# Kernel optimization log

Measured on AMD Instinct MI355X. Metric: run time of the kernel, lower is better.

The kernel has to match this reference:

```python
import jax, jax.numpy as jnp
import numpy as np

B, S, D, H = 8, 1024, 512, 8  # batch, max_mol_real, d_model, num_heads
DH = D // 2                   # per-branch width
DEPTH = D // H                # per-head depth (64)
HH = H // 2                   # heads per branch (4)


def setup_inputs() -> dict:
    key = jax.random.key(0)
    ks = jax.random.split(key, 16)
    sc = 0.02
    inp = {
        'x': jax.random.normal(ks[0], (B, S, D), jnp.float32),
        'mask': jnp.zeros((B, 1, 1, S), jnp.float32),
        'adj': jax.random.uniform(ks[1], (B, S, S), jnp.float32),
        'dist': jax.random.uniform(ks[2], (B, S, S), jnp.float32),
        # dist branch projections (Dense(d_model/2))
        'Wq_dist': jax.random.normal(ks[3], (D, DH), jnp.float32) * sc,
        'bq_dist': jnp.zeros((DH,), jnp.float32),
        'Wk_dist': jax.random.normal(ks[4], (D, DH), jnp.float32) * sc,
        'bk_dist': jnp.zeros((DH,), jnp.float32),
        'Wv_dist': jax.random.normal(ks[5], (D, DH), jnp.float32) * sc,
        'bv_dist': jnp.zeros((DH,), jnp.float32),
        # adj branch projections
        'Wq_adj': jax.random.normal(ks[6], (D, DH), jnp.float32) * sc,
        'bq_adj': jnp.zeros((DH,), jnp.float32),
        'Wk_adj': jax.random.normal(ks[7], (D, DH), jnp.float32) * sc,
        'bk_adj': jnp.zeros((DH,), jnp.float32),
        'Wv_adj': jax.random.normal(ks[8], (D, DH), jnp.float32) * sc,
        'bv_adj': jnp.zeros((DH,), jnp.float32),
        # output projection Dense(d_model)
        'Wo': jax.random.normal(ks[9], (D, D), jnp.float32) * sc,
        'bo': jnp.zeros((D,), jnp.float32),
    }
    return inp


def _split_heads(t):
    # (B, S, HH*DEPTH) -> (B, HH, S, DEPTH)
    return t.reshape(B, S, HH, DEPTH).transpose(0, 2, 1, 3)


def _sdpa_ad(q, k, v, mask, adj=None, dist=None):
    # mask: (B,1,1,S) -> additive -1e9 * mask, per original code
    m = mask * -1000000000.0
    logits = jnp.einsum('bhqd,bhkd->bhqk', q, k) / jnp.sqrt(jnp.float32(DEPTH))
    w = jax.nn.softmax(logits + m, axis=-1)  # (B, HH, S, S)
    if adj is not None:
        w = w * adj[:, None, :, :]
    if dist is not None:  # dist_value == 'original'
        w = w * jax.nn.softmax(dist[:, None, :, :] + m, axis=-1)
    return jnp.einsum('bhqk,bhkd->bhqd', w, v)


def reference(x, mask, adj, dist,
              Wq_dist, bq_dist, Wk_dist, bk_dist, Wv_dist, bv_dist,
              Wq_adj, bq_adj, Wk_adj, bk_adj, Wv_adj, bv_adj,
              Wo, bo):
    # ----- dist branch -----
    qd = _split_heads(x @ Wq_dist + bq_dist)
    kd = _split_heads(x @ Wk_dist + bk_dist)
    vd = _split_heads(x @ Wv_dist + bv_dist)
    od = _sdpa_ad(qd, kd, vd, mask, adj=None, dist=dist)
    od = od.transpose(0, 2, 1, 3).reshape(B, S, DH)
    # ----- adj branch -----
    qa = _split_heads(x @ Wq_adj + bq_adj)
    ka = _split_heads(x @ Wk_adj + bk_adj)
    va = _split_heads(x @ Wv_adj + bv_adj)
    oa = _sdpa_ad(qa, ka, va, mask, adj=adj, dist=None)
    oa = oa.transpose(0, 2, 1, 3).reshape(B, S, DH)
    # ----- concat + output dense -----
    cat = jnp.concatenate([od, oa], axis=-1)  # (B, S, D)
    return cat @ Wo + bo
```

## Files before the change

kernel.cpp:

```cpp
#include <hip/hip_runtime.h>

typedef __attribute__((ext_vector_type(8))) short bf16x8;
typedef __attribute__((ext_vector_type(4))) float f32x4;
typedef __attribute__((ext_vector_type(4))) unsigned u32x4;
typedef unsigned short ushortT;

#define B_   8
#define S_   1024
#define D_   512
#define DH_  256
#define NH_  4
#define DEP_ 64
#define LOG2E 1.4426950408889634f

__device__ __forceinline__ unsigned short f2bf(float f){
    unsigned u = __builtin_bit_cast(unsigned, f);
    u += 0x7fffu + ((u>>16)&1u);
    return (unsigned short)(u>>16);
}
__device__ __forceinline__ float bf2f(ushortT v){
    unsigned u = ((unsigned)v)<<16;
    return __builtin_bit_cast(float, u);
}
__device__ __forceinline__ unsigned fbits(float f){ return __builtin_bit_cast(unsigned, f); }
__device__ __forceinline__ int swz(int row,int cb){ return (row<<7) + (cb ^ ((row&7)<<4)); }
__device__ __forceinline__ int sigrow(int sr){
    return 16*((sr>>5) + 2*((sr>>2)&1)) + 4*((sr>>3)&3) + (sr&3);
}
__device__ __forceinline__ void gload_lds16(const void* g, void* l){
    __builtin_amdgcn_global_load_lds(
        (const __attribute__((address_space(1))) unsigned*)(size_t)g,
        (__attribute__((address_space(3))) unsigned*)(unsigned)(size_t)l,
        16, 0, 0);
}

__global__ __launch_bounds__(256) void mega_prep(
    const float* __restrict__ x, ushortT* __restrict__ xb,
    const float* __restrict__ W0, const float* __restrict__ W1, const float* __restrict__ W2,
    const float* __restrict__ W3, const float* __restrict__ W4, const float* __restrict__ W5,
    const float* __restrict__ B0, const float* __restrict__ B1, const float* __restrict__ B2,
    const float* __restrict__ B3, const float* __restrict__ B4, const float* __restrict__ B5,
    ushortT* __restrict__ Wt, float* __restrict__ bias_all,
    const float* __restrict__ dist, const float* __restrict__ mask, ushortT* __restrict__ Md)
{
    __shared__ ushortT pl[16][1032];
    const int bid = blockIdx.x;
    if (bid < 4096){
        size_t t = (size_t)bid*256 + threadIdx.x;
        float4 v = *(const float4*)(x + t*4);
        ushort4 o; o.x=f2bf(v.x); o.y=f2bf(v.y); o.z=f2bf(v.z); o.w=f2bf(v.w);
        *(ushort4*)(xb + t*4) = o;
        return;
    }
    if (bid < 4864){
        int t = (bid-4096)*256 + threadIdx.x;
        int k = t / 384;
        int n4 = (t - k*384)*4;
#pragma unroll
        for (int j=0;j<4;++j){
            int n = n4+j; int mat = n>>8, nc = n&255;
            const float* Wp = (mat==0)?W0:(mat==1)?W1:(mat==2)?W2:(mat==3)?W3:(mat==4)?W4:W5;
            Wt[(size_t)n*512 + k] = f2bf(Wp[(size_t)k*256 + nc]);
        }
        if (t < 384){
#pragma unroll
            for (int j=0;j<4;++j){
                int n = n4+j; int mat = n>>8, nc = n&255;
                const float* Bp = (mat==0)?B0:(mat==1)?B1:(mat==2)?B2:(mat==3)?B3:(mat==4)?B4:B5;
                bias_all[n] = Bp[nc];
            }
        }
        return;
    }
    const int bx = bid - 4864;
    const int w = bx&3, qb = (bx>>2)&15, b = bx>>6;
    const int wd = threadIdx.x>>6, lane = threadIdx.x&63;
    const float* mrow = mask + (size_t)b*S_;

    for (int rr=0; rr<4; ++rr){
        const int er = 4*wd + rr;
        const int q = qb*64 + 16*w + er;
        const float* drow = dist + ((size_t)(b*1024 + q))*S_;
        float v[16];
        float mx = -1e30f;
#pragma unroll
        for (int j=0;j<4;++j){
            const int idx = j*256 + lane*4;
            float4 d = *(const float4*)(drow + idx);
            float4 mk = *(const float4*)(mrow + idx);
            v[j*4+0] = fmaf(mk.x, -1e9f, d.x); v[j*4+1] = fmaf(mk.y, -1e9f, d.y);
            v[j*4+2] = fmaf(mk.z, -1e9f, d.z); v[j*4+3] = fmaf(mk.w, -1e9f, d.w);
#pragma unroll
            for (int i=0;i<4;++i) mx = fmaxf(mx, v[j*4+i]);
        }
        mx = fmaxf(mx, __shfl_xor(mx,1));  mx = fmaxf(mx, __shfl_xor(mx,2));
        mx = fmaxf(mx, __shfl_xor(mx,4));  mx = fmaxf(mx, __shfl_xor(mx,8));
        mx = fmaxf(mx, __shfl_xor(mx,16)); mx = fmaxf(mx, __shfl_xor(mx,32));
        float s = 0.f;
#pragma unroll
        for (int i=0;i<16;++i){ v[i] = __builtin_exp2f((v[i]-mx)*LOG2E); s += v[i]; }
        s += __shfl_xor(s,1);  s += __shfl_xor(s,2);  s += __shfl_xor(s,4);
        s += __shfl_xor(s,8);  s += __shfl_xor(s,16); s += __shfl_xor(s,32);
        const float rcp = 1.f/s;
#pragma unroll
        for (int j=0;j<4;++j){
            ushort4 o;
            o.x=f2bf(v[j*4+0]*rcp); o.y=f2bf(v[j*4+1]*rcp);
            o.z=f2bf(v[j*4+2]*rcp); o.w=f2bf(v[j*4+3]*rcp);
            *(ushort4*)(&pl[er][j*256 + lane*4]) = o;
        }
    }
    __syncthreads();

    const int t = threadIdx.x;
    const int e2 = (t>>2)&15, kt2 = t&3, g2 = t>>6;
    const int koff = 32*(kt2&1) + 4*(kt2>>1) + 8*g2;
    ushortT* slab = Md + (((size_t)(b*16+qb)*16)*4 + w)*1024;
#pragma unroll
    for (int s2=0;s2<16;++s2){
        ushort4 vv = *(const ushort4*)(&pl[e2][64*s2 + koff]);
        *(ushort4*)(slab + (size_t)s2*4096 + t*4) = vv;
    }
}

__global__ __launch_bounds__(256) void prep_wo(const float* __restrict__ Wo, ushortT* __restrict__ Wot){
    __shared__ float t[32][33];
    const int k0 = blockIdx.y*32, n0 = blockIdx.x*32;
    const int ty = threadIdx.x>>5, tx = threadIdx.x&31;
#pragma unroll
    for (int i=0;i<4;++i)
        t[ty+8*i][tx] = Wo[(size_t)(k0+ty+8*i)*512 + n0+tx];
    __syncthreads();
#pragma unroll
    for (int i=0;i<4;++i)
        Wot[(size_t)(n0+ty+8*i)*512 + k0+tx] = f2bf(t[tx][ty+8*i]);
}

__global__ __launch_bounds__(256) void shuf_adj(
    const float* __restrict__ adj, ushortT* __restrict__ Ma)
{
    __shared__ ushortT tl[64][72];
    const int bx = blockIdx.x;
    const int s = bx&15, qb = (bx>>4)&15, b = bx>>8;
    const int t = threadIdx.x;
    {
        const int qr = t>>2, c0 = (t&3)*16;
        const float* src = adj + ((size_t)(b*1024 + qb*64 + qr))*S_ + 64*s + c0;
#pragma unroll
        for (int i=0;i<4;++i){
            float4 d = *(const float4*)(src + 4*i);
            tl[qr][c0+4*i+0]=f2bf(d.x); tl[qr][c0+4*i+1]=f2bf(d.y);
            tl[qr][c0+4*i+2]=f2bf(d.z); tl[qr][c0+4*i+3]=f2bf(d.w);
        }
    }
    __syncthreads();
    const int w2 = t>>6, l = t&63, g = l>>4, e = l&15;
    ushortT o[16];
#pragma unroll
    for (int kt=0;kt<4;++kt)
        *(ushort4*)(&o[4*kt]) = *(const ushort4*)(&tl[16*w2 + e][32*(kt&1) + 4*(kt>>1) + 8*g]);
    ushortT* dst = Ma + ((((size_t)(b*16+qb)*16 + s)*4 + w2)*1024) + l*16;
    *(uint4*)(dst)     = *(uint4*)(&o[0]);
    *(uint4*)(dst + 8) = *(uint4*)(&o[8]);
}

__global__ __launch_bounds__(256) void qkv_mfma(
    const ushortT* __restrict__ xb, const ushortT* __restrict__ Wt,
    const float* __restrict__ bias_all,
    ushortT* __restrict__ q_d, ushortT* __restrict__ k_d, ushortT* __restrict__ vt_d,
    ushortT* __restrict__ q_a, ushortT* __restrict__ k_a, ushortT* __restrict__ vt_a)
{
    __shared__ __align__(16) char sm[32768];
    const int tid = threadIdx.x;
    const int w = tid>>6, l = tid&63, g = l>>4, e = l&15;
    const int wm = w>>1, wn = w&1;
    const int n0 = blockIdx.x*128, m0 = blockIdx.y*128;

    f32x4 acc[4][4];
#pragma unroll
    for (int i=0;i<4;++i)
#pragma unroll
        for (int j=0;j<4;++j) acc[i][j] = (f32x4){0.f,0.f,0.f,0.f};

    for (int k0=0;k0<512;k0+=64){
        __syncthreads();
#pragma unroll
        for (int i=0;i<4;++i){
            const int ch  = w*256 + i*64 + l;
            const int row = ch>>3;
            const int cb  = (ch&7)*16;
            const int gc  = (cb ^ ((row&7)<<4)) >> 1;
            gload_lds16(xb + (size_t)(m0+row)*512 + k0 + gc, sm + (w*4096 + i*1024));
            gload_lds16(Wt + (size_t)(n0+row)*512 + k0 + gc, sm + 16384 + (w*4096 + i*1024));
        }
        __syncthreads();
#pragma unroll
        for (int c=0;c<2;++c){
            bf16x8 a[4];
#pragma unroll
            for (int mt=0;mt<4;++mt)
                a[mt] = *(const bf16x8*)(sm + swz(64*wm + 16*mt + e, g*16 + 64*c));
#pragma unroll
            for (int nt=0;nt<4;++nt){
                bf16x8 bfr = *(const bf16x8*)(sm + 16384 + swz(64*wn + 16*nt + e, g*16 + 64*c));
#pragma unroll
                for (int mt=0;mt<4;++mt)
                    acc[mt][nt] = __builtin_amdgcn_mfma_f32_16x16x32_bf16(a[mt], bfr, acc[mt][nt], 0,0,0);
            }
        }
    }

    const int mat = n0>>8;
    const int nb  = n0 + 64*wn;
    const int h   = (nb&255)>>6;
    const int mb  = m0 + 64*wm;
    const int b   = mb>>10, s0 = mb&1023;
    ushortT* base = (mat==0)?q_d:(mat==1)?k_d:(mat==2)?vt_d:(mat==3)?q_a:(mat==4)?k_a:vt_a;
    const bool isV = (mat==2)||(mat==5);

    float bi[4];
#pragma unroll
    for (int nt=0;nt<4;++nt) bi[nt] = bias_all[nb + 16*nt + e];

    __syncthreads();
    char* qd = sm + w*8192;
#pragma unroll
    for (int nt=0;nt<4;++nt){
#pragma unroll
        for (int mt=0;mt<4;++mt){
#pragma unroll
            for (int r=0;r<4;++r){
                const int row = 16*mt + 4*g + r;
                const int col = 16*nt + e;
                const int lr = isV ? col : row;
                const int lc = isV ? row : col;
                *(ushortT*)(qd + swz(lr, lc*2)) = f2bf(acc[mt][nt][r] + bi[nt]);
            }
        }
    }
    const int rrb = l>>3, dq = l&7;
#pragma unroll
    for (int pass=0;pass<8;++pass){
        const int rr = pass*8 + rrb;
        uint4 vv = *(const uint4*)(qd + swz(rr, dq*16));
        const size_t off = isV ? ((size_t)((b*NH_+h)*DEP_ + rr)*S_ + s0 + dq*8)
                               : ((size_t)((b*NH_+h)*S_ + s0 + rr)*DEP_ + dq*8);
        *(uint4*)(base + off) = vv;
    }
}

__global__ __launch_bounds__(256,4) void attn_mfma(
    const ushortT* __restrict__ q_d, const ushortT* __restrict__ k_d, const ushortT* __restrict__ vt_d,
    const ushortT* __restrict__ q_a, const ushortT* __restrict__ k_a, const ushortT* __restrict__ vt_a,
    const ushortT* __restrict__ Md, const ushortT* __restrict__ Ma,
    const float* __restrict__ mask, ushortT* __restrict__ cat)
{
    __shared__ __align__(16) char sm[20480];
    float* Msk = (float*)(sm + 16384);

    const int tid = threadIdx.x;
    const int w = tid>>6, l = tid&63, g = l>>4, e = l&15;
    const int bz = blockIdx.y;
    const int br = bz>>5;
    const int bh = bz&31, b = bh>>2, h = bh&3;
    const int qb = blockIdx.x;
    const int q0 = qb*64;

    const ushortT* Qg = br ? q_a  : q_d;
    const ushortT* Kg = br ? k_a  : k_d;
    const ushortT* Vg = br ? vt_a : vt_d;

    const ushortT* Qb = Qg + ((size_t)bh*S_ + q0)*DEP_;
    const ushortT* Kb = Kg + (size_t)bh*S_*DEP_;
    const ushortT* Vb = Vg + (size_t)bh*DEP_*S_;
    const ushortT* Mbase = (br ? Ma : Md) + ((size_t)((b*16+qb)*16)*4 + w)*1024 + l*16;
    const float*   mkb = mask + (size_t)b*S_;

    const int srow = tid>>3, sf = tid&7;
    const int srow2 = srow+32;
    const int krow  = sigrow(srow);
    const int krow2 = sigrow(srow2);

    bf16x8 aq0 = *(const bf16x8*)(Qb + (size_t)(16*w+e)*DEP_ + 8*g);
    bf16x8 aq1 = *(const bf16x8*)(Qb + (size_t)(16*w+e)*DEP_ + 8*g + 32);

    for (int i=tid;i<S_;i+=256) Msk[i] = mkb[i] * (-1e9f*LOG2E);

    uint4 kreg0 = *(const uint4*)(Kb + (size_t)srow*DEP_ + 8*sf);
    uint4 kreg1 = *(const uint4*)(Kb + (size_t)srow2*DEP_ + 8*sf);
    uint4 vreg0 = *(const uint4*)(Vb + (size_t)srow*S_  + 8*sf);
    uint4 vreg1 = *(const uint4*)(Vb + (size_t)srow2*S_ + 8*sf);
    bf16x8 mc0 = *(const bf16x8*)(Mbase);
    bf16x8 mc1 = *(const bf16x8*)(Mbase + 8);

    float zl = 0.f;
    f32x4 oacc[4];
#pragma unroll
    for (int dt=0;dt<4;++dt) oacc[dt] = (f32x4){0.f,0.f,0.f,0.f};

    for (int s=0;s<16;++s){
        const int k0 = s*64;
        __syncthreads();
        *(uint4*)(sm +        swz(krow,  sf*16)) = kreg0;
        *(uint4*)(sm +        swz(krow2, sf*16)) = kreg1;
        *(uint4*)(sm + 8192 + swz(srow,  sf*16)) = vreg0;
        *(uint4*)(sm + 8192 + swz(srow2, sf*16)) = vreg1;
        __syncthreads();

        const int kn = (s<15) ? k0+64 : 0;
        kreg0 = *(const uint4*)(Kb + (size_t)(kn+srow)*DEP_ + 8*sf);
        kreg1 = *(const uint4*)(Kb + (size_t)(kn+srow2)*DEP_ + 8*sf);
        vreg0 = *(const uint4*)(Vb + (size_t)srow*S_  + kn + 8*sf);
        vreg1 = *(const uint4*)(Vb + (size_t)srow2*S_ + kn + 8*sf);
        const size_t mo = (size_t)((s<15)?s+1:0)*4096;
        bf16x8 mn0 = *(const bf16x8*)(Mbase + mo);
        bf16x8 mn1 = *(const bf16x8*)(Mbase + mo + 8);

        f32x4 lg[4];
#pragma unroll
        for (int kt=0;kt<4;++kt) lg[kt] = (f32x4){0.f,0.f,0.f,0.f};
        __builtin_amdgcn_s_setprio(1);
#pragma unroll
        for (int kt=0;kt<4;++kt){
            bf16x8 bk0 = *(const bf16x8*)(sm + swz(16*kt + e, g*16));
            bf16x8 bk1 = *(const bf16x8*)(sm + swz(16*kt + e, g*16 + 64));
            lg[kt] = __builtin_amdgcn_mfma_f32_16x16x32_bf16(bk0, aq0, lg[kt], 0,0,0);
            lg[kt] = __builtin_amdgcn_mfma_f32_16x16x32_bf16(bk1, aq1, lg[kt], 0,0,0);
        }
        __builtin_amdgcn_s_setprio(0);

        unsigned pw[8];
#pragma unroll
        for (int kt=0;kt<4;++kt){
            const f32x4 mskv = *(const f32x4*)(Msk + k0 + 32*(kt&1) + 4*(kt>>1) + 8*g);
            float e1[4], pm[4];
#pragma unroll
            for (int r=0;r<4;++r)
                e1[r] = __builtin_exp2f(fmaf(lg[kt][r], 0.125f*LOG2E, mskv[r]));
            zl += (e1[0]+e1[1]) + (e1[2]+e1[3]);
#pragma unroll
            for (int r=0;r<4;++r){
                const int j = 4*kt + r;
                const float mj = bf2f((ushortT)(j<8 ? mc0[j] : mc1[j-8]));
                pm[r] = e1[r]*mj;
            }
            pw[2*kt]   = __builtin_amdgcn_perm(fbits(pm[1]), fbits(pm[0]), 0x07060302u);
            pw[2*kt+1] = __builtin_amdgcn_perm(fbits(pm[3]), fbits(pm[2]), 0x07060302u);
        }
        mc0 = mn0; mc1 = mn1;

        const bf16x8 ap0 = __builtin_bit_cast(bf16x8, (u32x4){pw[0],pw[1],pw[4],pw[5]});
        const bf16x8 ap1 = __builtin_bit_cast(bf16x8, (u32x4){pw[2],pw[3],pw[6],pw[7]});

        __builtin_amdgcn_s_setprio(1);
#pragma unroll
        for (int dt=0;dt<4;++dt){
            bf16x8 bv0 = *(const bf16x8*)(sm + 8192 + swz(16*dt + e, g*16));
            oacc[dt] = __builtin_amdgcn_mfma_f32_16x16x32_bf16(ap0, bv0, oacc[dt], 0,0,0);
        }
#pragma unroll
        for (int dt=0;dt<4;++dt){
            bf16x8 bv1 = *(const bf16x8*)(sm + 8192 + swz(16*dt + e, g*16 + 64));
            oacc[dt] = __builtin_amdgcn_mfma_f32_16x16x32_bf16(ap1, bv1, oacc[dt], 0,0,0);
        }
        __builtin_amdgcn_s_setprio(0);
    }

    zl += __shfl_xor(zl,16); zl += __shfl_xor(zl,32);
    float inv[4];
#pragma unroll
    for (int r=0;r<4;++r)
        inv[r] = 1.f / __shfl(zl, (l & 48) | (4*g + r));

    const int coff = br*DH_;
#pragma unroll
    for (int dt=0;dt<4;++dt){
#pragma unroll
        for (int r=0;r<4;++r){
            int q = q0 + 16*w + 4*g + r;
            int c = coff + h*DEP_ + 16*dt + e;
            cat[((size_t)b*S_ + q)*D_ + c] = f2bf(oacc[dt][r]*inv[r]);
        }
    }
}

__global__ __launch_bounds__(256) void out_mfma(
    const ushortT* __restrict__ catb, const ushortT* __restrict__ Wot,
    const float* __restrict__ bo, float* __restrict__ out)
{
    __shared__ __align__(16) char sm[16384];
    const int tid = threadIdx.x;
    const int w = tid>>6, l = tid&63, g = l>>4, e = l&15;
    const int n0 = blockIdx.x*64, m0 = blockIdx.y*64;

    f32x4 acc[4];
#pragma unroll
    for (int j=0;j<4;++j) acc[j] = (f32x4){0.f,0.f,0.f,0.f};

    for (int k0=0;k0<512;k0+=64){
        __syncthreads();
#pragma unroll
        for (int i=0;i<2;++i){
            int fi = tid + i*256;
            int row = fi>>3, f = fi&7;
            *(uint4*)(sm + swz(row, f*16))        = *(const uint4*)(catb + ((size_t)(m0+row)*512 + k0 + 8*f));
            *(uint4*)(sm + 8192 + swz(row, f*16)) = *(const uint4*)(Wot  + ((size_t)(n0+row)*512 + k0 + 8*f));
        }
        __syncthreads();
#pragma unroll
        for (int c=0;c<2;++c){
            bf16x8 a = *(const bf16x8*)(sm + swz(16*w + e, g*16 + 64*c));
#pragma unroll
            for (int nt=0;nt<4;++nt){
                bf16x8 bfr = *(const bf16x8*)(sm + 8192 + swz(16*nt + e, g*16 + 64*c));
                acc[nt] = __builtin_amdgcn_mfma_f32_16x16x32_bf16(a, bfr, acc[nt], 0,0,0);
            }
        }
    }

#pragma unroll
    for (int nt=0;nt<4;++nt){
        const int n = n0 + 16*nt + e;
        const float bi = bo[n];
#pragma unroll
        for (int r=0;r<4;++r){
            const int m = m0 + 16*w + 4*g + r;
            out[(size_t)m*512 + n] = acc[nt][r] + bi;
        }
    }
}

extern "C" void kernel_launch(void* const* d_in, const int* in_sizes, int n_in,
                              void* d_out, int out_size, void* d_ws, size_t ws_size,
                              hipStream_t stream)
{
    (void)in_sizes; (void)n_in; (void)out_size; (void)ws_size;

    const float* x    = (const float*)d_in[0];
    const float* mask = (const float*)d_in[1];
    const float* adj  = (const float*)d_in[2];
    const float* dist = (const float*)d_in[3];
    const float* Wqd  = (const float*)d_in[4];  const float* bqd = (const float*)d_in[5];
    const float* Wkd  = (const float*)d_in[6];  const float* bkd = (const float*)d_in[7];
    const float* Wvd  = (const float*)d_in[8];  const float* bvd = (const float*)d_in[9];
    const float* Wqa  = (const float*)d_in[10]; const float* bqa = (const float*)d_in[11];
    const float* Wka  = (const float*)d_in[12]; const float* bka = (const float*)d_in[13];
    const float* Wva  = (const float*)d_in[14]; const float* bva = (const float*)d_in[15];
    const float* Wo   = (const float*)d_in[16]; const float* bo  = (const float*)d_in[17];
    float* out = (float*)d_out;

    char* W = (char*)d_ws;
    ushortT* xb   = (ushortT*)(W + 0);
    ushortT* catb = (ushortT*)(W + 0);
    ushortT* Wt   = (ushortT*)(W + 8388608);
    ushortT* Ma   = (ushortT*)(W + 8388608);
    ushortT* Wot  = (ushortT*)(W + 8388608);
    float*   bias = (float*)  (W + 9961472);
    ushortT* q_d  = (ushortT*)(W + 25165824);
    ushortT* k_d  = (ushortT*)(W + 29360128);
    ushortT* vt_d = (ushortT*)(W + 33554432);
    ushortT* q_a  = (ushortT*)(W + 37748736);
    ushortT* k_a  = (ushortT*)(W + 41943040);
    ushortT* vt_a = (ushortT*)(W + 46137344);
    ushortT* Md   = (ushortT*)(W + 50331648);

    mega_prep<<<5376, 256, 0, stream>>>(x, xb,
        Wqd,Wkd,Wvd,Wqa,Wka,Wva, bqd,bkd,bvd,bqa,bka,bva, Wt, bias,
        dist, mask, Md);
    qkv_mfma<<<dim3(12,64), 256, 0, stream>>>(xb, Wt, bias, q_d,k_d,vt_d, q_a,k_a,vt_a);
    shuf_adj<<<2048, 256, 0, stream>>>(adj, Ma);
    attn_mfma<<<dim3(16,64), 256, 0, stream>>>(q_d,k_d,vt_d, q_a,k_a,vt_a,
                                               Md, Ma, mask, catb);
    prep_wo<<<dim3(16,16), 256, 0, stream>>>(Wo, Wot);
    out_mfma<<<dim3(8,128), 256, 0, stream>>>(catb, Wot, bo, out);
}
```

Measured before the change: 113.3 us.

## Read adj directly as fp32 in attention and fold Wo transpose into prep

```diff
diff --git a/kernel.cpp b/kernel.cpp
--- a/kernel.cpp
+++ b/kernel.cpp
@@ -41,9 +41,11 @@
     const float* __restrict__ B0, const float* __restrict__ B1, const float* __restrict__ B2,
     const float* __restrict__ B3, const float* __restrict__ B4, const float* __restrict__ B5,
     ushortT* __restrict__ Wt, float* __restrict__ bias_all,
-    const float* __restrict__ dist, const float* __restrict__ mask, ushortT* __restrict__ Md)
+    const float* __restrict__ dist, const float* __restrict__ mask, ushortT* __restrict__ Md,
+    const float* __restrict__ Wo, ushortT* __restrict__ Wot)
 {
     __shared__ ushortT pl[16][1032];
+    __shared__ float tt[32][33];
     const int bid = blockIdx.x;
     if (bid < 4096){
         size_t t = (size_t)bid*256 + threadIdx.x;
@@ -72,96 +74,70 @@
         }
         return;
     }
-    const int bx = bid - 4864;
-    const int w = bx&3, qb = (bx>>2)&15, b = bx>>6;
-    const int wd = threadIdx.x>>6, lane = threadIdx.x&63;
-    const float* mrow = mask + (size_t)b*S_;
-
-    for (int rr=0; rr<4; ++rr){
-        const int er = 4*wd + rr;
-        const int q = qb*64 + 16*w + er;
-        const float* drow = dist + ((size_t)(b*1024 + q))*S_;
-        float v[16];
-        float mx = -1e30f;
-#pragma unroll
-        for (int j=0;j<4;++j){
-            const int idx = j*256 + lane*4;
-            float4 d = *(const float4*)(drow + idx);
-            float4 mk = *(const float4*)(mrow + idx);
-            v[j*4+0] = fmaf(mk.x, -1e9f, d.x); v[j*4+1] = fmaf(mk.y, -1e9f, d.y);
-            v[j*4+2] = fmaf(mk.z, -1e9f, d.z); v[j*4+3] = fmaf(mk.w, -1e9f, d.w);
-#pragma unroll
-            for (int i=0;i<4;++i) mx = fmaxf(mx, v[j*4+i]);
-        }
-        mx = fmaxf(mx, __shfl_xor(mx,1));  mx = fmaxf(mx, __shfl_xor(mx,2));
-        mx = fmaxf(mx, __shfl_xor(mx,4));  mx = fmaxf(mx, __shfl_xor(mx,8));
-        mx = fmaxf(mx, __shfl_xor(mx,16)); mx = fmaxf(mx, __shfl_xor(mx,32));
-        float s = 0.f;
-#pragma unroll
-        for (int i=0;i<16;++i){ v[i] = __builtin_exp2f((v[i]-mx)*LOG2E); s += v[i]; }
-        s += __shfl_xor(s,1);  s += __shfl_xor(s,2);  s += __shfl_xor(s,4);
-        s += __shfl_xor(s,8);  s += __shfl_xor(s,16); s += __shfl_xor(s,32);
-        const float rcp = 1.f/s;
-#pragma unroll
-        for (int j=0;j<4;++j){
-            ushort4 o;
-            o.x=f2bf(v[j*4+0]*rcp); o.y=f2bf(v[j*4+1]*rcp);
-            o.z=f2bf(v[j*4+2]*rcp); o.w=f2bf(v[j*4+3]*rcp);
-            *(ushort4*)(&pl[er][j*256 + lane*4]) = o;
-        }
-    }
-    __syncthreads();
-
-    const int t = threadIdx.x;
-    const int e2 = (t>>2)&15, kt2 = t&3, g2 = t>>6;
-    const int koff = 32*(kt2&1) + 4*(kt2>>1) + 8*g2;
-    ushortT* slab = Md + (((size_t)(b*16+qb)*16)*4 + w)*1024;
-#pragma unroll
-    for (int s2=0;s2<16;++s2){
-        ushort4 vv = *(const ushort4*)(&pl[e2][64*s2 + koff]);
-        *(ushort4*)(slab + (size_t)s2*4096 + t*4) = vv;
-    }
-}
-
-__global__ __launch_bounds__(256) void prep_wo(const float* __restrict__ Wo, ushortT* __restrict__ Wot){
-    __shared__ float t[32][33];
-    const int k0 = blockIdx.y*32, n0 = blockIdx.x*32;
-    const int ty = threadIdx.x>>5, tx = threadIdx.x&31;
-#pragma unroll
-    for (int i=0;i<4;++i)
-        t[ty+8*i][tx] = Wo[(size_t)(k0+ty+8*i)*512 + n0+tx];
-    __syncthreads();
-#pragma unroll
-    for (int i=0;i<4;++i)
-        Wot[(size_t)(n0+ty+8*i)*512 + k0+tx] = f2bf(t[tx][ty+8*i]);
-}
-
-__global__ __launch_bounds__(256) void shuf_adj(
-    const float* __restrict__ adj, ushortT* __restrict__ Ma)
-{
-    __shared__ ushortT tl[64][72];
-    const int bx = blockIdx.x;
-    const int s = bx&15, qb = (bx>>4)&15, b = bx>>8;
-    const int t = threadIdx.x;
+    if (bid < 5376){
+        const int bx = bid - 4864;
+        const int w = bx&3, qb = (bx>>2)&15, b = bx>>6;
+        const int wd = threadIdx.x>>6, lane = threadIdx.x&63;
+        const float* mrow = mask + (size_t)b*S_;
+
+        for (int rr=0; rr<4; ++rr){
+            const int er = 4*wd + rr;
+            const int q = qb*64 + 16*w + er;
+            const float* drow = dist + ((size_t)(b*1024 + q))*S_;
+            float v[16];
+            float mx = -1e30f;
+#pragma unroll
+            for (int j=0;j<4;++j){
+                const int idx = j*256 + lane*4;
+                float4 d = *(const float4*)(drow + idx);
+                float4 mk = *(const float4*)(mrow + idx);
+                v[j*4+0] = fmaf(mk.x, -1e9f, d.x); v[j*4+1] = fmaf(mk.y, -1e9f, d.y);
+                v[j*4+2] = fmaf(mk.z, -1e9f, d.z); v[j*4+3] = fmaf(mk.w, -1e9f, d.w);
+#pragma unroll
+                for (int i=0;i<4;++i) mx = fmaxf(mx, v[j*4+i]);
+            }
+            mx = fmaxf(mx, __shfl_xor(mx,1));  mx = fmaxf(mx, __shfl_xor(mx,2));
+            mx = fmaxf(mx, __shfl_xor(mx,4));  mx = fmaxf(mx, __shfl_xor(mx,8));
+            mx = fmaxf(mx, __shfl_xor(mx,16)); mx = fmaxf(mx, __shfl_xor(mx,32));
+            float s = 0.f;
+#pragma unroll
+            for (int i=0;i<16;++i){ v[i] = __builtin_exp2f((v[i]-mx)*LOG2E); s += v[i]; }
+            s += __shfl_xor(s,1);  s += __shfl_xor(s,2);  s += __shfl_xor(s,4);
+            s += __shfl_xor(s,8);  s += __shfl_xor(s,16); s += __shfl_xor(s,32);
+            const float rcp = 1.f/s;
+#pragma unroll
+            for (int j=0;j<4;++j){
+                ushort4 o;
+                o.x=f2bf(v[j*4+0]*rcp); o.y=f2bf(v[j*4+1]*rcp);
+                o.z=f2bf(v[j*4+2]*rcp); o.w=f2bf(v[j*4+3]*rcp);
+                *(ushort4*)(&pl[er][j*256 + lane*4]) = o;
+            }
+        }
+        __syncthreads();
+
+        const int t = threadIdx.x;
+        const int e2 = (t>>2)&15, kt2 = t&3, g2 = t>>6;
+        const int koff = 32*(kt2&1) + 4*(kt2>>1) + 8*g2;
+        ushortT* slab = Md + (((size_t)(b*16+qb)*16)*4 + w)*1024;
+#pragma unroll
+        for (int s2=0;s2<16;++s2){
+            ushort4 vv = *(const ushort4*)(&pl[e2][64*s2 + koff]);
+            *(ushort4*)(slab + (size_t)s2*4096 + t*4) = vv;
+        }
+        return;
+    }
     {
-        const int qr = t>>2, c0 = (t&3)*16;
-        const float* src = adj + ((size_t)(b*1024 + qb*64 + qr))*S_ + 64*s + c0;
-#pragma unroll
-        for (int i=0;i<4;++i){
-            float4 d = *(const float4*)(src + 4*i);
-            tl[qr][c0+4*i+0]=f2bf(d.x); tl[qr][c0+4*i+1]=f2bf(d.y);
-            tl[qr][c0+4*i+2]=f2bf(d.z); tl[qr][c0+4*i+3]=f2bf(d.w);
-        }
-    }
-    __syncthreads();
-    const int w2 = t>>6, l = t&63, g = l>>4, e = l&15;
-    ushortT o[16];
-#pragma unroll
-    for (int kt=0;kt<4;++kt)
-        *(ushort4*)(&o[4*kt]) = *(const ushort4*)(&tl[16*w2 + e][32*(kt&1) + 4*(kt>>1) + 8*g]);
-    ushortT* dst = Ma + ((((size_t)(b*16+qb)*16 + s)*4 + w2)*1024) + l*16;
-    *(uint4*)(dst)     = *(uint4*)(&o[0]);
-    *(uint4*)(dst + 8) = *(uint4*)(&o[8]);
+        const int bid2 = bid - 5376;
+        const int n0 = (bid2 & 15)*32, k0 = (bid2 >> 4)*32;
+        const int ty = threadIdx.x>>5, tx = threadIdx.x&31;
+#pragma unroll
+        for (int i=0;i<4;++i)
+            tt[ty+8*i][tx] = Wo[(size_t)(k0+ty+8*i)*512 + n0+tx];
+        __syncthreads();
+#pragma unroll
+        for (int i=0;i<4;++i)
+            Wot[(size_t)(n0+ty+8*i)*512 + k0+tx] = f2bf(tt[tx][ty+8*i]);
+    }
 }
 
 __global__ __launch_bounds__(256) void qkv_mfma(
@@ -252,7 +228,7 @@
 __global__ __launch_bounds__(256,4) void attn_mfma(
     const ushortT* __restrict__ q_d, const ushortT* __restrict__ k_d, const ushortT* __restrict__ vt_d,
     const ushortT* __restrict__ q_a, const ushortT* __restrict__ k_a, const ushortT* __restrict__ vt_a,
-    const ushortT* __restrict__ Md, const ushortT* __restrict__ Ma,
+    const ushortT* __restrict__ Md, const float* __restrict__ adj,
     const float* __restrict__ mask, ushortT* __restrict__ cat)
 {
     __shared__ __align__(16) char sm[20480];
@@ -273,7 +249,8 @@
     const ushortT* Qb = Qg + ((size_t)bh*S_ + q0)*DEP_;
     const ushortT* Kb = Kg + (size_t)bh*S_*DEP_;
     const ushortT* Vb = Vg + (size_t)bh*DEP_*S_;
-    const ushortT* Mbase = (br ? Ma : Md) + ((size_t)((b*16+qb)*16)*4 + w)*1024 + l*16;
+    const ushortT* Mbase = Md + ((size_t)((b*16+qb)*16)*4 + w)*1024 + l*16;
+    const float*   Ab    = adj + (size_t)(b*S_ + q0 + 16*w + e)*S_ + 8*g;
     const float*   mkb = mask + (size_t)b*S_;
 
     const int srow = tid>>3, sf = tid&7;
@@ -290,8 +267,16 @@
     uint4 kreg1 = *(const uint4*)(Kb + (size_t)srow2*DEP_ + 8*sf);
     uint4 vreg0 = *(const uint4*)(Vb + (size_t)srow*S_  + 8*sf);
     uint4 vreg1 = *(const uint4*)(Vb + (size_t)srow2*S_ + 8*sf);
-    bf16x8 mc0 = *(const bf16x8*)(Mbase);
-    bf16x8 mc1 = *(const bf16x8*)(Mbase + 8);
+    bf16x8 mc0, mc1;
+    f32x4  mcf[4];
+    if (br==0){
+        mc0 = *(const bf16x8*)(Mbase);
+        mc1 = *(const bf16x8*)(Mbase + 8);
+    } else {
+#pragma unroll
+        for (int kt=0;kt<4;++kt)
+            mcf[kt] = *(const f32x4*)(Ab + 32*(kt&1) + 4*(kt>>1));
+    }
 
     float zl = 0.f;
     f32x4 oacc[4];
@@ -312,9 +297,17 @@
         kreg1 = *(const uint4*)(Kb + (size_t)(kn+srow2)*DEP_ + 8*sf);
         vreg0 = *(const uint4*)(Vb + (size_t)srow*S_  + kn + 8*sf);
         vreg1 = *(const uint4*)(Vb + (size_t)srow2*S_ + kn + 8*sf);
-        const size_t mo = (size_t)((s<15)?s+1:0)*4096;
-        bf16x8 mn0 = *(const bf16x8*)(Mbase + mo);
-        bf16x8 mn1 = *(const bf16x8*)(Mbase + mo + 8);
+        bf16x8 mn0, mn1;
+        f32x4  mnf[4];
+        if (br==0){
+            const size_t mo = (size_t)((s<15)?s+1:0)*4096;
+            mn0 = *(const bf16x8*)(Mbase + mo);
+            mn1 = *(const bf16x8*)(Mbase + mo + 8);
+        } else {
+#pragma unroll
+            for (int kt=0;kt<4;++kt)
+                mnf[kt] = *(const f32x4*)(Ab + kn + 32*(kt&1) + 4*(kt>>1));
+        }
 
         f32x4 lg[4];
 #pragma unroll
@@ -341,13 +334,18 @@
 #pragma unroll
             for (int r=0;r<4;++r){
                 const int j = 4*kt + r;
-                const float mj = bf2f((ushortT)(j<8 ? mc0[j] : mc1[j-8]));
+                const float mj = (br==0) ? bf2f((ushortT)(j<8 ? mc0[j] : mc1[j-8]))
+                                         : mcf[kt][r];
                 pm[r] = e1[r]*mj;
             }
             pw[2*kt]   = __builtin_amdgcn_perm(fbits(pm[1]), fbits(pm[0]), 0x07060302u);
             pw[2*kt+1] = __builtin_amdgcn_perm(fbits(pm[3]), fbits(pm[2]), 0x07060302u);
         }
-        mc0 = mn0; mc1 = mn1;
+        if (br==0){ mc0 = mn0; mc1 = mn1; }
+        else {
+#pragma unroll
+            for (int kt=0;kt<4;++kt) mcf[kt] = mnf[kt];
+        }
 
         const bf16x8 ap0 = __builtin_bit_cast(bf16x8, (u32x4){pw[0],pw[1],pw[4],pw[5]});
         const bf16x8 ap1 = __builtin_bit_cast(bf16x8, (u32x4){pw[2],pw[3],pw[6],pw[7]});
@@ -453,9 +451,8 @@
     ushortT* xb   = (ushortT*)(W + 0);
     ushortT* catb = (ushortT*)(W + 0);
     ushortT* Wt   = (ushortT*)(W + 8388608);
-    ushortT* Ma   = (ushortT*)(W + 8388608);
-    ushortT* Wot  = (ushortT*)(W + 8388608);
     float*   bias = (float*)  (W + 9961472);
+    ushortT* Wot  = (ushortT*)(W + 10485760);
     ushortT* q_d  = (ushortT*)(W + 25165824);
     ushortT* k_d  = (ushortT*)(W + 29360128);
     ushortT* vt_d = (ushortT*)(W + 33554432);
@@ -464,13 +461,11 @@
     ushortT* vt_a = (ushortT*)(W + 46137344);
     ushortT* Md   = (ushortT*)(W + 50331648);
 
-    mega_prep<<<5376, 256, 0, stream>>>(x, xb,
+    mega_prep<<<5632, 256, 0, stream>>>(x, xb,
         Wqd,Wkd,Wvd,Wqa,Wka,Wva, bqd,bkd,bvd,bqa,bka,bva, Wt, bias,
-        dist, mask, Md);
+        dist, mask, Md, Wo, Wot);
     qkv_mfma<<<dim3(12,64), 256, 0, stream>>>(xb, Wt, bias, q_d,k_d,vt_d, q_a,k_a,vt_a);
-    shuf_adj<<<2048, 256, 0, stream>>>(adj, Ma);
     attn_mfma<<<dim3(16,64), 256, 0, stream>>>(q_d,k_d,vt_d, q_a,k_a,vt_a,
-                                               Md, Ma, mask, catb);
-    prep_wo<<<dim3(16,16), 256, 0, stream>>>(Wo, Wot);
+                                               Md, adj, mask, catb);
     out_mfma<<<dim3(8,128), 256, 0, stream>>>(catb, Wot, bo, out);
 }
```

New measurement: 212.3 us. 87.4% more time.
